# Performance work log

Hardware: AMD Instinct MI355X
Metric: run time of the kernel (lower is better)

The kernel has to match this reference:

```python
import jax, jax.numpy as jnp
import numpy as np
import math

# ---- static config (must match init_kwargs / input_specs) ----
D = 1024
N_HEAD = 16
HEAD_DIM = D // N_HEAD          # 64
HALF = HEAD_DIM // 2            # rope half dim = 32
N_EXP = 8
TOP_K = 2
CAP_FACTOR = 2.0
LN_EPS = 1e-5


def _build_sin_cos(T, half_dim, dtype=jnp.float32):
    pos = jnp.arange(T, dtype=dtype)[:, None]                      # (T,1)
    inv_freq = 1.0 / (10000.0 ** (jnp.arange(0, 2 * half_dim, 2, dtype=dtype) / (2 * half_dim)))
    ang = pos * inv_freq[None, :]                                  # (T, half)
    return jnp.sin(ang), jnp.cos(ang)


def _layernorm(x, g, b):
    mu = jnp.mean(x, axis=-1, keepdims=True)
    var = jnp.mean(jnp.square(x - mu), axis=-1, keepdims=True)
    return (x - mu) * jax.lax.rsqrt(var + LN_EPS) * g + b


def _apply_rope(q, k, sin, cos):
    # q,k: (B,T,H,hd); sin,cos: (T, half)
    s = sin[None, :, None, :]
    c = cos[None, :, None, :]
    q1, q2 = q[..., :HALF], q[..., HALF:]
    k1, k2 = k[..., :HALF], k[..., HALF:]
    qr = jnp.concatenate([q1 * c - q2 * s, q1 * s + q2 * c], axis=-1)
    kr = jnp.concatenate([k1 * c - k2 * s, k1 * s + k2 * c], axis=-1)
    return qr, kr


def _attention(x, Wqkv, Wproj):
    B, T, C = x.shape
    qkv = x @ Wqkv                                                  # (B,T,3C)
    qkv = qkv.reshape(B, T, N_HEAD, 3 * HEAD_DIM)
    q, k, v = jnp.split(qkv, 3, axis=-1)                            # each (B,T,H,hd)
    sin, cos = _build_sin_cos(T, HALF)
    q, k = _apply_rope(q, k, sin, cos)
    scale = 1.0 / math.sqrt(HEAD_DIM)
    att = jnp.einsum('bqhd,bkhd->bhqk', q, k) * scale               # (B,H,T,T)
    causal = jnp.tril(jnp.ones((T, T), dtype=bool))
    att = jnp.where(causal[None, None], att, jnp.finfo(att.dtype).min)
    p = jax.nn.softmax(att, axis=-1)
    o = jnp.einsum('bhqk,bkhd->bqhd', p, v).reshape(B, T, C)
    return o @ Wproj, k, v


def _sparse_moe(flat, Wgate, W1, b1, W2, b2):
    # flat: (N, d). Eval mode: no router noise.
    N, d = flat.shape
    capacity = int(math.ceil(CAP_FACTOR * N / N_EXP))
    logits = flat @ Wgate                                           # (N,E)
    gates = jax.nn.softmax(logits, axis=-1)
    vals, inds = jax.lax.top_k(gates, TOP_K)                        # (N,k)
    flat_inds = inds.reshape(-1)                                    # (N*k,)
    flat_vals = vals.reshape(-1)
    neg = jnp.finfo(flat.dtype).min
    # per-expert assignment scores over all (token, slot) pairs
    scores = jnp.where(flat_inds[None, :] == jnp.arange(N_EXP)[:, None],
                       flat_vals[None, :], neg)                     # (E, N*k)
    top_scores, top_pos = jax.lax.top_k(scores, capacity)           # (E, cap)
    tok_idx = top_pos // TOP_K                                      # (E, cap)
    w = jnp.where(top_scores > neg, top_scores, 0.0)                # dropped slots -> 0 weight
    xe = flat[tok_idx]                                              # gather: (E, cap, d)
    h = jax.nn.gelu(jnp.einsum('ecd,edh->ech', xe, W1) + b1[:, None, :], approximate=False)
    out = jnp.einsum('ech,ehd->ecd', h, W2) + b2[:, None, :]
    out = out * w[..., None]
    final = jnp.zeros_like(flat).at[tok_idx.reshape(-1)].add(out.reshape(-1, d))
    return final


def setup_inputs() -> dict:
    key = jax.random.key(0)
    ks = jax.random.split(key, 10)
    B, T = 2, 2048
    s = 0.02
    return {
        'x': jax.random.normal(ks[0], (B, T, D), dtype=jnp.float32),
        'ln1_g': jnp.ones((D,), jnp.float32),
        'ln1_b': jnp.zeros((D,), jnp.float32),
        'ln2_g': jnp.ones((D,), jnp.float32),
        'ln2_b': jnp.zeros((D,), jnp.float32),
        'Wqkv': jax.random.normal(ks[1], (D, 3 * D), jnp.float32) * s,
        'Wproj': jax.random.normal(ks[2], (D, D), jnp.float32) * s,
        'Wgate': jax.random.normal(ks[3], (D, N_EXP), jnp.float32) * s,
        'W1': jax.random.normal(ks[4], (N_EXP, D, 4 * D), jnp.float32) * s,
        'b1': jnp.zeros((N_EXP, 4 * D), jnp.float32),
        'W2': jax.random.normal(ks[5], (N_EXP, 4 * D, D), jnp.float32) * s,
        'b2': jnp.zeros((N_EXP, D), jnp.float32),
    }


def reference(x, ln1_g, ln1_b, ln2_g, ln2_b, Wqkv, Wproj, Wgate, W1, b1, W2, b2):
    B, T, _ = x.shape
    x_norm = _layernorm(x, ln1_g, ln1_b)
    attn_out, k, v = _attention(x_norm, Wqkv, Wproj)
    x = x + attn_out
    ff_in = _layernorm(x, ln2_g, ln2_b)
    moe_out = _sparse_moe(ff_in.reshape(B * T, D), Wgate, W1, b1, W2, b2)
    x = x + moe_out.reshape(B, T, D)
    aux_loss = jnp.zeros((), x.dtype)  # eval mode
    return x, aux_loss, k, v
```

## Files before the change

kernel.cpp:

```cpp
#include <hip/hip_runtime.h>
#include <hip/hip_bf16.h>
#include <math.h>


#define TT 2048
#define NTOK 4096

typedef __attribute__((ext_vector_type(8))) short bf16x8;
typedef __attribute__((ext_vector_type(4))) float f32x4;
typedef __attribute__((ext_vector_type(16))) float f32x16;

static __device__ __forceinline__ ushort f2bf(float f) {
  union { float f; unsigned u; } v; v.f = f;
  unsigned r = v.u + 0x7FFFu + ((v.u >> 16) & 1u);
  return (ushort)(r >> 16);
}
static __device__ __forceinline__ float bf2f(ushort h) {
  union { unsigned u; float f; } v; v.u = ((unsigned)h) << 16; return v.f;
}
static __device__ __forceinline__ unsigned cvt_pk_bf16(float lo, float hi) {
  unsigned r;
  asm("v_cvt_pk_bf16_f32 %0, %1, %2" : "=v"(r) : "v"(lo), "v"(hi));
  return r;
}
static __device__ __forceinline__ void plane_swap(unsigned& a, unsigned& b) {
  asm("v_permlane32_swap_b32 %0, %1" : "+v"(a), "+v"(b));
}

template<bool WF32>
__global__ __launch_bounds__(256)
void ln_kernel(const float* __restrict__ x, const float* __restrict__ g,
               const float* __restrict__ b, float* __restrict__ out,
               ushort* __restrict__ oh, ushort* __restrict__ ol) {
  int row = blockIdx.x, tid = threadIdx.x;
  const float4* xr = (const float4*)(x + (size_t)row * 1024);
  float4 v = xr[tid];
  float s = v.x + v.y + v.z + v.w;
  #pragma unroll
  for (int off = 1; off < 64; off <<= 1) s += __shfl_xor(s, off);
  __shared__ float red1[4], red2[4];
  if ((tid & 63) == 0) red1[tid >> 6] = s;
  __syncthreads();
  float mu = (red1[0] + red1[1] + red1[2] + red1[3]) * (1.0f / 1024.0f);
  float dx = v.x - mu, dy = v.y - mu, dz = v.z - mu, dw = v.w - mu;
  float ss = dx*dx + dy*dy + dz*dz + dw*dw;
  #pragma unroll
  for (int off = 1; off < 64; off <<= 1) ss += __shfl_xor(ss, off);
  if ((tid & 63) == 0) red2[tid >> 6] = ss;
  __syncthreads();
  float var = (red2[0] + red2[1] + red2[2] + red2[3]) * (1.0f / 1024.0f);
  float inv = 1.0f / sqrtf(var + 1e-5f);
  float4 g4 = ((const float4*)g)[tid];
  float4 b4 = ((const float4*)b)[tid];
  float4 o4;
  o4.x = dx * inv * g4.x + b4.x;
  o4.y = dy * inv * g4.y + b4.y;
  o4.z = dz * inv * g4.z + b4.z;
  o4.w = dw * inv * g4.w + b4.w;
  if constexpr (WF32)
    ((float4*)(out + (size_t)row * 1024))[tid] = o4;
  size_t base = (size_t)row * 1024 + tid * 4;
  ushort h0 = f2bf(o4.x), h1 = f2bf(o4.y), h2 = f2bf(o4.z), h3 = f2bf(o4.w);
  ushort4 hh = {h0, h1, h2, h3};
  *(ushort4*)(oh + base) = hh;
  ushort4 ll = {f2bf(o4.x - bf2f(h0)), f2bf(o4.y - bf2f(h1)),
                f2bf(o4.z - bf2f(h2)), f2bf(o4.w - bf2f(h3))};
  *(ushort4*)(ol + base) = ll;
}

__global__ void sincos_kernel(float* __restrict__ st, float* __restrict__ ct) {
  int t = blockIdx.x, j = threadIdx.x;
  double invf = pow(10000.0, -((double)(2 * j)) / 64.0);
  double ang = (double)t * invf;
  st[t * 32 + j] = (float)sin(ang);
  ct[t * 32 + j] = (float)cos(ang);
}

__global__ __launch_bounds__(256)
void rope_kernel(float* __restrict__ qkv, const float* __restrict__ st,
                 const float* __restrict__ ct, float* __restrict__ kout,
                 float* __restrict__ vout, ushort* __restrict__ Kh,
                 ushort* __restrict__ Kl) {
  int row = blockIdx.x;
  int t = row & (TT - 1);
  int b = row >> 11;
  int tid = threadIdx.x;
  float* base = qkv + (size_t)row * 3072;
  #pragma unroll
  for (int l = 0; l < 2; ++l) {
    int idx = l * 256 + tid;
    int h = idx >> 5, j = idx & 31;
    float s = st[t * 32 + j], c = ct[t * 32 + j];
    float* qp = base + h * 192;
    float q1 = qp[j], q2 = qp[j + 32];
    qp[j]      = q1 * c - q2 * s;
    qp[j + 32] = q1 * s + q2 * c;
    float k1 = qp[64 + j], k2 = qp[96 + j];
    float kr1 = k1 * c - k2 * s, kr2 = k1 * s + k2 * c;
    qp[64 + j] = kr1; qp[96 + j] = kr2;
    kout[(size_t)row * 1024 + h * 64 + j]      = kr1;
    kout[(size_t)row * 1024 + h * 64 + 32 + j] = kr2;
    size_t kb = ((size_t)(b * 16 + h) * TT + t) * 64;
    ushort h1 = f2bf(kr1);
    Kh[kb + j] = h1; Kl[kb + j] = f2bf(kr1 - bf2f(h1));
    ushort h2 = f2bf(kr2);
    Kh[kb + 32 + j] = h2; Kl[kb + 32 + j] = f2bf(kr2 - bf2f(h2));
  }
  #pragma unroll
  for (int l = 0; l < 4; ++l) {
    int f = l * 256 + tid;
    int h = f >> 6, d = f & 63;
    vout[(size_t)row * 1024 + f] = base[h * 192 + 128 + d];
  }
}

__global__ __launch_bounds__(256)
void vtprep_kernel(const float* __restrict__ vout, ushort* __restrict__ Vth,
                   ushort* __restrict__ Vtl) {
  __shared__ float tile[64][65];
  int t0 = blockIdx.x * 64, h = blockIdx.y, b = blockIdx.z;
  int tid = threadIdx.x;
  #pragma unroll
  for (int l = 0; l < 4; ++l) {
    int idx = l * 256 + tid;
    int r = idx >> 4, c4 = (idx & 15) * 4;
    *(float4*)&tile[r][c4] = *(const float4*)&vout[((size_t)(b * TT + t0 + r)) * 1024 + h * 64 + c4];
  }
  __syncthreads();
  int d = tid >> 2, ts = (tid & 3) * 16;
  union { bf16x8 v; ushort u[8]; } H0, H1, L0, L1;
  #pragma unroll
  for (int i = 0; i < 8; ++i) {
    float v0 = tile[ts + i][d];
    ushort hb0 = f2bf(v0);
    H0.u[i] = hb0; L0.u[i] = f2bf(v0 - bf2f(hb0));
    float v1 = tile[ts + 8 + i][d];
    ushort hb1 = f2bf(v1);
    H1.u[i] = hb1; L1.u[i] = f2bf(v1 - bf2f(hb1));
  }
  size_t basep = ((size_t)(b * 16 + h) * 64 + d) * TT + t0 + ts;
  *(bf16x8*)(Vth + basep) = H0.v;  *(bf16x8*)(Vth + basep + 8) = H1.v;
  *(bf16x8*)(Vtl + basep) = L0.v;  *(bf16x8*)(Vtl + basep + 8) = L1.v;
}

__global__ __launch_bounds__(256)
void flash7_kernel(const float* __restrict__ qkv, const ushort* __restrict__ Kh,
                   const ushort* __restrict__ Kl, const ushort* __restrict__ Vth,
                   const ushort* __restrict__ Vtl, float* __restrict__ Opart,
                   float* __restrict__ Mpart, float* __restrict__ Lpart) {
  const int offt[16] = {0,1,2,4,6,9,12,16,20,25,30,36,42,49,56,64};
  int lin = blockIdx.x;
  int xcd = lin & 7, s = lin >> 3;
  int bh = xcd + 8 * (s / 72);
  int j = 71 - (s % 72);
  int qt = 0, off = 0;
  #pragma unroll
  for (int u = 0; u < 16; ++u)
    if (j >= offt[u]) { qt = u; off = offt[u]; }
  int kc = j - off;
  int slot = bh * 72 + j;
  int h = bh & 15, b = bh >> 4;
  int tid = threadIdx.x;
  int w = tid >> 6, lane = tid & 63;
  int q = lane & 31, LH = lane >> 5;
  size_t bT = (size_t)b * TT;
  int qglob0 = qt * 128 + w * 32;
  int qg = qglob0 + q;
  bf16x8 qH[4], qL[4];
  {
    const float* qp = qkv + (bT + qg) * 3072 + h * 192 + LH * 8;
    #pragma unroll
    for (int dblk = 0; dblk < 4; ++dblk) {
      float4 f0 = *(const float4*)(qp + dblk * 16);
      float4 f1 = *(const float4*)(qp + dblk * 16 + 4);
      float vals[8] = {f0.x, f0.y, f0.z, f0.w, f1.x, f1.y, f1.z, f1.w};
      union { bf16x8 v; ushort u[8]; } H, L;
      #pragma unroll
      for (int e = 0; e < 8; ++e) {
        ushort hb = f2bf(vals[e]);
        H.u[e] = hb; L.u[e] = f2bf(vals[e] - bf2f(hb));
      }
      qH[dblk] = H.v; qL[dblk] = L.v;
    }
  }
  const ushort* Kbh = Kh + (size_t)bh * TT * 64;
  const ushort* Kbl = Kl + (size_t)bh * TT * 64;
  const ushort* Vbh = Vth + (size_t)bh * 64 * TT;
  const ushort* Vbl = Vtl + (size_t)bh * 64 * TT;
  f32x16 accO0 = {}, accO1 = {};
  float m = -3.402823466e38f, lsum = 0.0f;
  int kvlo = kc * 256;
  int kvhi = min(kvlo + 256, qglob0 + 32);

  for (int kv0 = kvlo; kv0 < kvhi; kv0 += 32) {
    const ushort* kbh = Kbh + (size_t)(kv0 + q) * 64 + LH * 8;
    const ushort* kbl = Kbl + (size_t)(kv0 + q) * 64 + LH * 8;
    bf16x8 kAH[4], kAL[4];
    #pragma unroll
    for (int dblk = 0; dblk < 4; ++dblk) {
      kAH[dblk] = *(const bf16x8*)(kbh + dblk * 16);
      kAL[dblk] = *(const bf16x8*)(kbl + dblk * 16);
    }
    f32x16 sa = {}, sb = {};
    __builtin_amdgcn_s_setprio(1);
    sa = __builtin_amdgcn_mfma_f32_32x32x16_bf16(kAH[0], qH[0], sa, 0, 0, 0);
    sb = __builtin_amdgcn_mfma_f32_32x32x16_bf16(kAH[2], qH[2], sb, 0, 0, 0);
    sa = __builtin_amdgcn_mfma_f32_32x32x16_bf16(kAH[1], qH[1], sa, 0, 0, 0);
    sb = __builtin_amdgcn_mfma_f32_32x32x16_bf16(kAH[3], qH[3], sb, 0, 0, 0);
    sa = __builtin_amdgcn_mfma_f32_32x32x16_bf16(kAH[0], qL[0], sa, 0, 0, 0);
    sb = __builtin_amdgcn_mfma_f32_32x32x16_bf16(kAH[2], qL[2], sb, 0, 0, 0);
    sa = __builtin_amdgcn_mfma_f32_32x32x16_bf16(kAH[1], qL[1], sa, 0, 0, 0);
    sb = __builtin_amdgcn_mfma_f32_32x32x16_bf16(kAH[3], qL[3], sb, 0, 0, 0);
    sa = __builtin_amdgcn_mfma_f32_32x32x16_bf16(kAL[0], qH[0], sa, 0, 0, 0);
    sb = __builtin_amdgcn_mfma_f32_32x32x16_bf16(kAL[2], qH[2], sb, 0, 0, 0);
    sa = __builtin_amdgcn_mfma_f32_32x32x16_bf16(kAL[1], qH[1], sa, 0, 0, 0);
    sb = __builtin_amdgcn_mfma_f32_32x32x16_bf16(kAL[3], qH[3], sb, 0, 0, 0);
    __builtin_amdgcn_s_setprio(0);
    bf16x8 vAH[2][2], vAL[2][2];
    #pragma unroll
    for (int dblk = 0; dblk < 2; ++dblk)
      #pragma unroll
      for (int s2 = 0; s2 < 2; ++s2) {
        size_t ad = (size_t)(dblk * 32 + q) * TT + kv0 + s2 * 16 + LH * 8;
        vAH[dblk][s2] = *(const bf16x8*)(Vbh + ad);
        vAL[dblk][s2] = *(const bf16x8*)(Vbl + ad);
      }
    float p[16];
    float pmax = -3.402823466e38f;
    if (kv0 + 31 > qglob0) {
      #pragma unroll
      for (int r = 0; r < 16; ++r) {
        int kvg = kv0 + (r & 3) + 8 * (r >> 2) + 4 * LH;
        float sv = (kvg <= qg) ? (sa[r] + sb[r]) * 0.125f : -3.402823466e38f;
        p[r] = sv; pmax = fmaxf(pmax, sv);
      }
    } else {
      #pragma unroll
      for (int r = 0; r < 16; ++r) {
        float sv = (sa[r] + sb[r]) * 0.125f;
        p[r] = sv; pmax = fmaxf(pmax, sv);
      }
    }
    pmax = fmaxf(pmax, __shfl_xor(pmax, 32));
    float mnew = fmaxf(m, pmax);
    float fsc = __expf(m - mnew);
    float psum = 0.0f;
    #pragma unroll
    for (int r = 0; r < 16; ++r) { p[r] = __expf(p[r] - mnew); psum += p[r]; }
    psum += __shfl_xor(psum, 32);
    lsum = lsum * fsc + psum;
    m = mnew;
    #pragma unroll
    for (int r = 0; r < 16; ++r) { accO0[r] *= fsc; accO1[r] *= fsc; }
    bf16x8 pHf[2], pLf[2];
    #pragma unroll
    for (int s2 = 0; s2 < 2; ++s2) {
      int s8 = s2 * 8;
      unsigned a  = cvt_pk_bf16(p[s8 + 0], p[s8 + 1]);
      unsigned bw = cvt_pk_bf16(p[s8 + 2], p[s8 + 3]);
      unsigned c  = cvt_pk_bf16(p[s8 + 4], p[s8 + 5]);
      unsigned d  = cvt_pk_bf16(p[s8 + 6], p[s8 + 7]);
      float l0 = p[s8 + 0] - __uint_as_float(a << 16);
      float l1 = p[s8 + 1] - __uint_as_float(a & 0xFFFF0000u);
      float l2 = p[s8 + 2] - __uint_as_float(bw << 16);
      float l3 = p[s8 + 3] - __uint_as_float(bw & 0xFFFF0000u);
      float l4 = p[s8 + 4] - __uint_as_float(c << 16);
      float l5 = p[s8 + 5] - __uint_as_float(c & 0xFFFF0000u);
      float l6 = p[s8 + 6] - __uint_as_float(d << 16);
      float l7 = p[s8 + 7] - __uint_as_float(d & 0xFFFF0000u);
      unsigned al = cvt_pk_bf16(l0, l1);
      unsigned bl = cvt_pk_bf16(l2, l3);
      unsigned cl = cvt_pk_bf16(l4, l5);
      unsigned dl = cvt_pk_bf16(l6, l7);
      plane_swap(a, c); plane_swap(bw, d);
      plane_swap(al, cl); plane_swap(bl, dl);
      union { unsigned w[4]; bf16x8 v; } PH, PL;
      PH.w[0] = a;  PH.w[1] = bw; PH.w[2] = c;  PH.w[3] = d;
      PL.w[0] = al; PL.w[1] = bl; PL.w[2] = cl; PL.w[3] = dl;
      pHf[s2] = PH.v; pLf[s2] = PL.v;
    }
    __builtin_amdgcn_s_setprio(1);
    #pragma unroll
    for (int s2 = 0; s2 < 2; ++s2) {
      accO0 = __builtin_amdgcn_mfma_f32_32x32x16_bf16(vAH[0][s2], pHf[s2], accO0, 0, 0, 0);
      accO1 = __builtin_amdgcn_mfma_f32_32x32x16_bf16(vAH[1][s2], pHf[s2], accO1, 0, 0, 0);
      accO0 = __builtin_amdgcn_mfma_f32_32x32x16_bf16(vAH[0][s2], pLf[s2], accO0, 0, 0, 0);
      accO1 = __builtin_amdgcn_mfma_f32_32x32x16_bf16(vAH[1][s2], pLf[s2], accO1, 0, 0, 0);
      accO0 = __builtin_amdgcn_mfma_f32_32x32x16_bf16(vAL[0][s2], pHf[s2], accO0, 0, 0, 0);
      accO1 = __builtin_amdgcn_mfma_f32_32x32x16_bf16(vAL[1][s2], pHf[s2], accO1, 0, 0, 0);
    }
    __builtin_amdgcn_s_setprio(0);
  }
  if (LH == 0) {
    Mpart[slot * 128 + w * 32 + q] = m;
    Lpart[slot * 128 + w * 32 + q] = lsum;
  }
  float* Ob = Opart + (size_t)slot * 8192 + (w * 32 + q) * 64;
  #pragma unroll
  for (int g2 = 0; g2 < 4; ++g2) {
    float4 v0 = {accO0[g2 * 4 + 0], accO0[g2 * 4 + 1], accO0[g2 * 4 + 2], accO0[g2 * 4 + 3]};
    *(float4*)(Ob + 8 * g2 + 4 * LH) = v0;
    float4 v1 = {accO1[g2 * 4 + 0], accO1[g2 * 4 + 1], accO1[g2 * 4 + 2], accO1[g2 * 4 + 3]};
    *(float4*)(Ob + 32 + 8 * g2 + 4 * LH) = v1;
  }
}

__global__ __launch_bounds__(256)
void fmerge2_kernel(const float* __restrict__ Opart, const float* __restrict__ Mpart,
                    const float* __restrict__ Lpart, ushort* __restrict__ oh,
                    ushort* __restrict__ ol) {
  const int offt[16] = {0,1,2,4,6,9,12,16,20,25,30,36,42,49,56,64};
  int qt = blockIdx.x, bh = blockIdx.y;
  int h = bh & 15, b = bh >> 4;
  int nc = (qt + 2) >> 1;
  int slot0 = bh * 72 + offt[qt];
  int tid = threadIdx.x;
  int q = tid & 127, dh = tid >> 7;
  float mg = -3.402823466e38f;
  for (int c = 0; c < nc; ++c) mg = fmaxf(mg, Mpart[(slot0 + c) * 128 + q]);
  float lg = 0.0f;
  float4 acc[8] = {};
  for (int c = 0; c < nc; ++c) {
    float sc = __expf(Mpart[(slot0 + c) * 128 + q] - mg);
    lg += sc * Lpart[(slot0 + c) * 128 + q];
    const float4* op = (const float4*)(Opart + (size_t)(slot0 + c) * 8192 + q * 64 + dh * 32);
    #pragma unroll
    for (int i = 0; i < 8; ++i) {
      float4 v = op[i];
      acc[i].x += sc * v.x; acc[i].y += sc * v.y;
      acc[i].z += sc * v.z; acc[i].w += sc * v.w;
    }
  }
  float inv = 1.0f / lg;
  size_t obase = ((size_t)(b * TT + qt * 128 + q)) * 1024 + h * 64 + dh * 32;
  #pragma unroll
  for (int i = 0; i < 8; ++i) {
    float4 v = {acc[i].x * inv, acc[i].y * inv, acc[i].z * inv, acc[i].w * inv};
    ushort h0 = f2bf(v.x), h1 = f2bf(v.y), h2 = f2bf(v.z), h3 = f2bf(v.w);
    ushort4 hh = {h0, h1, h2, h3};
    *(ushort4*)(oh + obase + i * 4) = hh;
    ushort4 ll = {f2bf(v.x - bf2f(h0)), f2bf(v.y - bf2f(h1)),
                  f2bf(v.z - bf2f(h2)), f2bf(v.w - bf2f(h3))};
    *(ushort4*)(ol + obase + i * 4) = ll;
  }
}

template<bool LO>
__global__ void tconv_kernel(const float* __restrict__ in, ushort* __restrict__ oh,
                             ushort* __restrict__ ol, int K, int N) {
  __shared__ float t[32][33];
  int z = blockIdx.z;
  const float* ip = in + (size_t)z * K * N;
  ushort* ohp = oh + (size_t)z * K * N;
  ushort* olp = LO ? (ol + (size_t)z * K * N) : nullptr;
  int n0 = blockIdx.x * 32, k0 = blockIdx.y * 32;
  int tx = threadIdx.x, ty = threadIdx.y;
  #pragma unroll
  for (int i = 0; i < 4; ++i)
    t[ty + 8 * i][tx] = ip[(size_t)(k0 + ty + 8 * i) * N + n0 + tx];
  __syncthreads();
  #pragma unroll
  for (int i = 0; i < 4; ++i) {
    float v = t[tx][ty + 8 * i];
    size_t off = (size_t)(n0 + ty + 8 * i) * K + k0 + tx;
    ushort hb = f2bf(v);
    ohp[off] = hb;
    if (LO) olp[off] = f2bf(v - bf2f(hb));
  }
}

#define LOAD_STEP(tt) do {                                                     \
    int seg = SPLIT3 ? ((tt) / kPer) : 0;                                      \
    int kk = (SPLIT3 ? ((tt) % kPer) : (tt)) << 6;                             \
    const ushort* Ause = (SPLIT3 && seg == 2) ? AlB : AhB;                     \
    const ushort* Buse = (SPLIT3 && seg == 1) ? BlB : BhB;                     \
    _Pragma("unroll")                                                          \
    for (int q = 0; q < 4; ++q) {                                              \
      int rr = r0 + 32 * q;                                                    \
      int clog = cph ^ (rr & 7);                                               \
      ra[q] = *(const bf16x8*)(Ause + (size_t)garow[q] * K + kk + clog * 8);   \
      rb[q] = *(const bf16x8*)(Buse + (size_t)(bn + rr) * K + kk + clog * 8);  \
    }                                                                          \
  } while (0)

template<int EPI, bool GATHER, bool SPLIT3>
__global__ __launch_bounds__(256, 2)
void mgemm(const ushort* __restrict__ Ah, const ushort* __restrict__ Al,
           const ushort* __restrict__ Bh, const ushort* __restrict__ Bl,
           void* __restrict__ Cv, const float* __restrict__ extra,
           const int* __restrict__ gatAll, int N, int K,
           long aEStride, long bEStride, long cEStride, int biasEStride) {
  __shared__ ushort As[128 * 64];
  __shared__ ushort Bs[128 * 64];
  int z = blockIdx.z;
  const ushort* AhB = Ah + (size_t)z * aEStride;
  const ushort* AlB = SPLIT3 ? (Al + (size_t)z * aEStride) : nullptr;
  const ushort* BhB = Bh + (size_t)z * bEStride;
  const ushort* BlB = SPLIT3 ? (Bl + (size_t)z * bEStride) : nullptr;
  const int* gat = GATHER ? (gatAll + z * 1024) : nullptr;
  int bm = blockIdx.y * 128, bn = blockIdx.x * 128;
  int tid = threadIdx.x;
  int r0 = tid >> 3, cph = tid & 7;
  int garow[4];
  #pragma unroll
  for (int q = 0; q < 4; ++q) {
    int rr = r0 + 32 * q;
    garow[q] = GATHER ? gat[bm + rr] : (bm + rr);
  }
  int kPer = K >> 6;
  int kSteps = (SPLIT3 ? 3 : 1) * kPer;
  int wid = tid >> 6, lane = tid & 63;
  int wm = wid >> 1, wn = wid & 1;
  int lr = lane & 15, lk = lane >> 4;
  f32x4 acc[4][4] = {};
  bf16x8 ra[4], rb[4];
  LOAD_STEP(0);
  for (int t = 0; t < kSteps; ++t) {
    __syncthreads();
    #pragma unroll
    for (int q = 0; q < 4; ++q) {
      int rr = r0 + 32 * q;
      *(bf16x8*)&As[rr * 64 + cph * 8] = ra[q];
      *(bf16x8*)&Bs[rr * 64 + cph * 8] = rb[q];
    }
    __syncthreads();
    if (t + 1 < kSteps) LOAD_STEP(t + 1);
    #pragma unroll
    for (int kh = 0; kh < 2; ++kh) {
      bf16x8 af[4], bfr[4];
      #pragma unroll
      for (int mf = 0; mf < 4; ++mf) {
        int row = wm * 64 + mf * 16 + lr;
        int ch = (kh * 4 + lk) ^ (row & 7);
        af[mf] = *(const bf16x8*)&As[row * 64 + ch * 8];
      }
      #pragma unroll
      for (int nf = 0; nf < 4; ++nf) {
        int row = wn * 64 + nf * 16 + lr;
        int ch = (kh * 4 + lk) ^ (row & 7);
        bfr[nf] = *(const bf16x8*)&Bs[row * 64 + ch * 8];
      }
      #pragma unroll
      for (int mf = 0; mf < 4; ++mf)
        #pragma unroll
        for (int nf = 0; nf < 4; ++nf)
          acc[mf][nf] = __builtin_amdgcn_mfma_f32_16x16x32_bf16(af[mf], bfr[nf], acc[mf][nf], 0, 0, 0);
    }
  }
  int crow = bm + wm * 64, ccol = bn + wn * 64;
  if constexpr (EPI <= 1) {
    float* C = (float*)Cv;
    #pragma unroll
    for (int mf = 0; mf < 4; ++mf)
      #pragma unroll
      for (int nf = 0; nf < 4; ++nf)
        #pragma unroll
        for (int r = 0; r < 4; ++r) {
          int row = crow + mf * 16 + lk * 4 + r;
          int col = ccol + nf * 16 + lr;
          float v = acc[mf][nf][r];
          if constexpr (EPI == 1) v += extra[(size_t)row * N + col];
          C[(size_t)row * N + col] = v;
        }
  } else {
    const float* bias = extra + (size_t)z * biasEStride;
    ushort* C = (ushort*)Cv + (size_t)z * cEStride;
    #pragma unroll
    for (int mf = 0; mf < 4; ++mf)
      #pragma unroll
      for (int nf = 0; nf < 4; ++nf)
        #pragma unroll
        for (int r = 0; r < 4; ++r) {
          int row = crow + mf * 16 + lk * 4 + r;
          int col = ccol + nf * 16 + lr;
          float v = acc[mf][nf][r] + bias[col];
          if constexpr (EPI == 2)
            v = 0.5f * v * (1.0f + erff(v * 0.70710678118654752f));
          C[(size_t)row * N + col] = f2bf(v);
        }
  }
}

__global__ __launch_bounds__(256)
void gate_kernel(const float* __restrict__ ffin, const float* __restrict__ Wg,
                 int* __restrict__ te, float* __restrict__ tv, int* __restrict__ inv) {
  int token = blockIdx.x, tid = threadIdx.x;
  float acc[8] = {};
  const float* xr = ffin + (size_t)token * 1024;
  for (int i = tid; i < 1024; i += 256) {
    float xv = xr[i];
    const float4* wr = (const float4*)&Wg[i * 8];
    float4 w0 = wr[0], w1 = wr[1];
    acc[0] += xv * w0.x; acc[1] += xv * w0.y; acc[2] += xv * w0.z; acc[3] += xv * w0.w;
    acc[4] += xv * w1.x; acc[5] += xv * w1.y; acc[6] += xv * w1.z; acc[7] += xv * w1.w;
  }
  #pragma unroll
  for (int off = 1; off < 64; off <<= 1)
    #pragma unroll
    for (int q = 0; q < 8; ++q) acc[q] += __shfl_xor(acc[q], off);
  __shared__ float red[4][8];
  if ((tid & 63) == 0)
    #pragma unroll
    for (int q = 0; q < 8; ++q) red[tid >> 6][q] = acc[q];
  __syncthreads();
  if (tid == 0) {
    float g[8];
    #pragma unroll
    for (int q = 0; q < 8; ++q) g[q] = red[0][q] + red[1][q] + red[2][q] + red[3][q];
    float mx = g[0];
    #pragma unroll
    for (int q = 1; q < 8; ++q) mx = fmaxf(mx, g[q]);
    float sum = 0.0f;
    #pragma unroll
    for (int q = 0; q < 8; ++q) { g[q] = expf(g[q] - mx); sum += g[q]; }
    float inv_s = 1.0f / sum;
    #pragma unroll
    for (int q = 0; q < 8; ++q) g[q] *= inv_s;
    int e1 = 0; float v1 = g[0];
    for (int q = 1; q < 8; ++q) if (g[q] > v1) { v1 = g[q]; e1 = q; }
    int e2 = -1; float v2 = -1.0f;
    for (int q = 0; q < 8; ++q) { if (q == e1) continue; if (g[q] > v2) { v2 = g[q]; e2 = q; } }
    te[token * 2] = e1; te[token * 2 + 1] = e2;
    tv[token * 2] = v1; tv[token * 2 + 1] = v2;
    inv[token * 2] = -1; inv[token * 2 + 1] = -1;
  }
}

__global__ __launch_bounds__(1024)
void route_sort_kernel(const int* __restrict__ te, const float* __restrict__ tv,
                       int* __restrict__ etok, float* __restrict__ ew,
                       int* __restrict__ inv) {
  __shared__ unsigned long long sk[4096];
  __shared__ int wcnt[16];
  __shared__ int base;
  int e = blockIdx.x, tid = threadIdx.x;
  int lane = tid & 63, wv = tid >> 6;
  if (tid == 0) base = 0;
  __syncthreads();
  for (int c = 0; c < 8; ++c) {
    int s = c * 1024 + tid;
    bool sel = (te[s] == e);
    unsigned long long ball = __ballot(sel);
    int pre = __popcll(ball & ((1ull << lane) - 1ull));
    if (lane == 0) wcnt[wv] = __popcll(ball);
    __syncthreads();
    int woff = 0, tot = 0;
    #pragma unroll
    for (int i = 0; i < 16; ++i) {
      int cc = wcnt[i];
      if (i < wv) woff += cc;
      tot += cc;
    }
    if (sel) {
      unsigned vb = __float_as_uint(tv[s]);
      sk[base + woff + pre] =
          ((unsigned long long)vb << 32) | (unsigned)(0xFFFFFFFFu - (unsigned)s);
    }
    __syncthreads();
    if (tid == 0) base += tot;
    __syncthreads();
  }
  int n = base;
  if (n > 1024) {
    int P = (n <= 2048) ? 2048 : 4096;
    for (int i = n + tid; i < P; i += 1024) sk[i] = 0ull;
    __syncthreads();
    for (int k = 2; k <= P; k <<= 1)
      for (int j = k >> 1; j > 0; j >>= 1) {
        for (int t = tid; t < (P >> 1); t += 1024) {
          int i = ((t & ~(j - 1)) << 1) | (t & (j - 1));
          int p = i | j;
          unsigned long long a = sk[i], bq = sk[p];
          bool desc = ((i & k) == 0);
          if (desc ? (a < bq) : (a > bq)) { sk[i] = bq; sk[p] = a; }
        }
        __syncthreads();
      }
  }
  int cap = n < 1024 ? n : 1024;
  if (tid < cap) {
    unsigned long long key = sk[tid];
    unsigned slot = 0xFFFFFFFFu - (unsigned)(key & 0xFFFFFFFFull);
    etok[e * 1024 + tid] = (int)(slot >> 1);
    ew[e * 1024 + tid] = __uint_as_float((unsigned)(key >> 32));
    inv[slot] = e * 1024 + tid;
  } else {
    etok[e * 1024 + tid] = 0;
    ew[e * 1024 + tid] = 0.0f;
  }
}

__global__ __launch_bounds__(256)
void combine_kernel(const float* __restrict__ xres, const ushort* __restrict__ eo,
                    const int* __restrict__ inv, const float* __restrict__ ew,
                    float* __restrict__ outx, float* __restrict__ aux) {
  int token = blockIdx.x;
  int d = threadIdx.x * 4;
  float4 acc = *(const float4*)&xres[(size_t)token * 1024 + d];
  #pragma unroll
  for (int j = 0; j < 2; ++j) {
    int p = inv[token * 2 + j];
    if (p >= 0) {
      float w = ew[p];
      const ushort* ep = eo + (size_t)p * 1024 + d;
      acc.x += w * bf2f(ep[0]); acc.y += w * bf2f(ep[1]);
      acc.z += w * bf2f(ep[2]); acc.w += w * bf2f(ep[3]);
    }
  }
  *(float4*)&outx[(size_t)token * 1024 + d] = acc;
  if (token == 0 && threadIdx.x == 0) aux[0] = 0.0f;
}

extern "C" void kernel_launch(void* const* d_in, const int* in_sizes, int n_in,
                              void* d_out, int out_size, void* d_ws, size_t ws_size,
                              hipStream_t stream) {
  const float* x     = (const float*)d_in[0];
  const float* ln1g  = (const float*)d_in[1];
  const float* ln1b  = (const float*)d_in[2];
  const float* ln2g  = (const float*)d_in[3];
  const float* ln2b  = (const float*)d_in[4];
  const float* Wqkv  = (const float*)d_in[5];
  const float* Wproj = (const float*)d_in[6];
  const float* Wg    = (const float*)d_in[7];
  const float* W1    = (const float*)d_in[8];
  const float* b1    = (const float*)d_in[9];
  const float* W2    = (const float*)d_in[10];
  const float* b2    = (const float*)d_in[11];

  float* out_x   = (float*)d_out;
  float* out_aux = out_x + 4194304;
  float* out_k   = out_aux + 1;
  float* out_v   = out_k + 4194304;

  float* ws   = (float*)d_ws;
  float* A    = ws;
  float* qkvb = ws + 4194304;
  float* o    = ws + 16777216;
  float* st   = ws + 20971520;
  float* ct   = ws + 21037056;
  int*   te   = (int*)(ws + 21102592);
  float* tv   = ws + 21110784;
  int*   etok = (int*)(ws + 21118976);
  float* ew   = ws + 21127168;
  int*   inv  = (int*)(ws + 21135360);
  ushort* bfAh = (ushort*)(ws + 21143552);
  ushort* bfAl = (ushort*)(ws + 23240704);
  ushort* BqH  = (ushort*)(ws + 25337856);
  ushort* BqL  = (ushort*)(ws + 26910720);
  ushort* BpH  = (ushort*)(ws + 28483584);
  ushort* BpL  = (ushort*)(ws + 29007872);
  ushort* W1t  = (ushort*)(ws + 29532160);
  ushort* W2t  = (ushort*)(ws + 46309376);
  ushort* eo   = (ushort*)(ws + 63086592);
  ushort* hbuf = (ushort*)(ws + 4194304);
  ushort* Kh_  = bfAh;
  ushort* Kl_  = bfAl;
  ushort* Vth_ = eo;
  ushort* Vtl_ = eo + 4194304;
  float* Opart = ws + 29532160;
  float* Mpart = ws + 48406528;
  float* Lpart = ws + 48701440;

  tconv_kernel<true ><<<dim3(96, 32, 1),  dim3(32, 8), 0, stream>>>(Wqkv,  BqH, BqL, 1024, 3072);
  tconv_kernel<true ><<<dim3(32, 32, 1),  dim3(32, 8), 0, stream>>>(Wproj, BpH, BpL, 1024, 1024);
  sincos_kernel<<<TT, 32, 0, stream>>>(st, ct);

  ln_kernel<false><<<NTOK, 256, 0, stream>>>(x, ln1g, ln1b, nullptr, bfAh, bfAl);
  mgemm<0, false, true><<<dim3(24, 32, 1), 256, 0, stream>>>(
      bfAh, bfAl, BqH, BqL, qkvb, nullptr, nullptr, 3072, 1024, 0, 0, 0, 0);
  rope_kernel<<<NTOK, 256, 0, stream>>>(qkvb, st, ct, out_k, out_v, Kh_, Kl_);
  vtprep_kernel<<<dim3(32, 16, 2), 256, 0, stream>>>(out_v, Vth_, Vtl_);
  flash7_kernel<<<2304, 256, 0, stream>>>(qkvb, Kh_, Kl_, Vth_, Vtl_, Opart, Mpart, Lpart);
  fmerge2_kernel<<<dim3(16, 32), 256, 0, stream>>>(Opart, Mpart, Lpart, bfAh, bfAl);
  mgemm<1, false, true><<<dim3(8, 32, 1), 256, 0, stream>>>(
      bfAh, bfAl, BpH, BpL, A, x, nullptr, 1024, 1024, 0, 0, 0, 0);
  tconv_kernel<false><<<dim3(128, 32, 8), dim3(32, 8), 0, stream>>>(W1, W1t, nullptr, 1024, 4096);
  tconv_kernel<false><<<dim3(32, 128, 8), dim3(32, 8), 0, stream>>>(W2, W2t, nullptr, 4096, 1024);
  ln_kernel<true><<<NTOK, 256, 0, stream>>>(A, ln2g, ln2b, o, bfAh, bfAl);
  gate_kernel<<<NTOK, 256, 0, stream>>>(o, Wg, te, tv, inv);
  route_sort_kernel<<<8, 1024, 0, stream>>>(te, tv, etok, ew, inv);
  mgemm<2, true, false><<<dim3(32, 8, 8), 256, 0, stream>>>(
      bfAh, nullptr, W1t, nullptr, hbuf, b1, etok, 4096, 1024,
      0, 4096L * 1024, 1024L * 4096, 4096);
  mgemm<3, false, false><<<dim3(8, 8, 8), 256, 0, stream>>>(
      hbuf, nullptr, W2t, nullptr, eo, b2, nullptr, 1024, 4096,
      1024L * 4096, 1024L * 4096, 1024L * 1024, 1024);
  combine_kernel<<<NTOK, 256, 0, stream>>>(A, eo, inv, ew, out_x, out_aux);
}
```

Measured before the change: 704.0 us.

## Fuse MoE gate into second layernorm and software-pipeline K loads in flash attention

The router gate computation (logits, softmax, top-2) moves into the second layernorm kernel, working on the normalized row held in shared memory. This removes the fp32 layernorm output write, its re-read and one kernel launch. The flash kernel now prefetches the next K tile into a second register set while the current tile's MFMAs run, and folds the 1/sqrt(d) scale into Q before bf16 splitting. This costs extra registers and may lower occupancy, and pre-scaling Q changes rounding slightly (0.125 is exact, so the effect should be small).

```diff
diff --git a/kernel.cpp b/kernel.cpp
--- a/kernel.cpp
+++ b/kernel.cpp
@@ -27,11 +27,13 @@
   asm("v_permlane32_swap_b32 %0, %1" : "+v"(a), "+v"(b));
 }
 
-template<bool WF32>
+template<bool GATE>
 __global__ __launch_bounds__(256)
 void ln_kernel(const float* __restrict__ x, const float* __restrict__ g,
-               const float* __restrict__ b, float* __restrict__ out,
-               ushort* __restrict__ oh, ushort* __restrict__ ol) {
+               const float* __restrict__ b, ushort* __restrict__ oh,
+               ushort* __restrict__ ol, const float* __restrict__ Wg,
+               int* __restrict__ te, float* __restrict__ tv, int* __restrict__ inv) {
+  __shared__ float srow[1024];
   int row = blockIdx.x, tid = threadIdx.x;
   const float4* xr = (const float4*)(x + (size_t)row * 1024);
   float4 v = xr[tid];
@@ -49,16 +51,14 @@
   if ((tid & 63) == 0) red2[tid >> 6] = ss;
   __syncthreads();
   float var = (red2[0] + red2[1] + red2[2] + red2[3]) * (1.0f / 1024.0f);
-  float inv = 1.0f / sqrtf(var + 1e-5f);
+  float inv_ = 1.0f / sqrtf(var + 1e-5f);
   float4 g4 = ((const float4*)g)[tid];
   float4 b4 = ((const float4*)b)[tid];
   float4 o4;
-  o4.x = dx * inv * g4.x + b4.x;
-  o4.y = dy * inv * g4.y + b4.y;
-  o4.z = dz * inv * g4.z + b4.z;
-  o4.w = dw * inv * g4.w + b4.w;
-  if constexpr (WF32)
-    ((float4*)(out + (size_t)row * 1024))[tid] = o4;
+  o4.x = dx * inv_ * g4.x + b4.x;
+  o4.y = dy * inv_ * g4.y + b4.y;
+  o4.z = dz * inv_ * g4.z + b4.z;
+  o4.w = dw * inv_ * g4.w + b4.w;
   size_t base = (size_t)row * 1024 + tid * 4;
   ushort h0 = f2bf(o4.x), h1 = f2bf(o4.y), h2 = f2bf(o4.z), h3 = f2bf(o4.w);
   ushort4 hh = {h0, h1, h2, h3};
@@ -66,6 +66,48 @@
   ushort4 ll = {f2bf(o4.x - bf2f(h0)), f2bf(o4.y - bf2f(h1)),
                 f2bf(o4.z - bf2f(h2)), f2bf(o4.w - bf2f(h3))};
   *(ushort4*)(ol + base) = ll;
+  if constexpr (GATE) {
+    *(float4*)&srow[tid * 4] = o4;
+    __syncthreads();
+    float acc[8] = {};
+    for (int i = tid; i < 1024; i += 256) {
+      float xv = srow[i];
+      const float4* wr = (const float4*)&Wg[i * 8];
+      float4 w0 = wr[0], w1 = wr[1];
+      acc[0] += xv * w0.x; acc[1] += xv * w0.y; acc[2] += xv * w0.z; acc[3] += xv * w0.w;
+      acc[4] += xv * w1.x; acc[5] += xv * w1.y; acc[6] += xv * w1.z; acc[7] += xv * w1.w;
+    }
+    #pragma unroll
+    for (int off = 1; off < 64; off <<= 1)
+      #pragma unroll
+      for (int qq = 0; qq < 8; ++qq) acc[qq] += __shfl_xor(acc[qq], off);
+    __shared__ float red[4][8];
+    if ((tid & 63) == 0)
+      #pragma unroll
+      for (int qq = 0; qq < 8; ++qq) red[tid >> 6][qq] = acc[qq];
+    __syncthreads();
+    if (tid == 0) {
+      float gg[8];
+      #pragma unroll
+      for (int qq = 0; qq < 8; ++qq) gg[qq] = red[0][qq] + red[1][qq] + red[2][qq] + red[3][qq];
+      float mx = gg[0];
+      #pragma unroll
+      for (int qq = 1; qq < 8; ++qq) mx = fmaxf(mx, gg[qq]);
+      float sum = 0.0f;
+      #pragma unroll
+      for (int qq = 0; qq < 8; ++qq) { gg[qq] = expf(gg[qq] - mx); sum += gg[qq]; }
+      float inv_s = 1.0f / sum;
+      #pragma unroll
+      for (int qq = 0; qq < 8; ++qq) gg[qq] *= inv_s;
+      int e1 = 0; float v1 = gg[0];
+      for (int qq = 1; qq < 8; ++qq) if (gg[qq] > v1) { v1 = gg[qq]; e1 = qq; }
+      int e2 = -1; float v2 = -1.0f;
+      for (int qq = 0; qq < 8; ++qq) { if (qq == e1) continue; if (gg[qq] > v2) { v2 = gg[qq]; e2 = qq; } }
+      te[row * 2] = e1; te[row * 2 + 1] = e2;
+      tv[row * 2] = v1; tv[row * 2 + 1] = v2;
+      inv[row * 2] = -1; inv[row * 2 + 1] = -1;
+    }
+  }
 }
 
 __global__ void sincos_kernel(float* __restrict__ st, float* __restrict__ ct) {
@@ -144,7 +186,7 @@
 }
 
 __global__ __launch_bounds__(256)
-void flash7_kernel(const float* __restrict__ qkv, const ushort* __restrict__ Kh,
+void flash8_kernel(const float* __restrict__ qkv, const ushort* __restrict__ Kh,
                    const ushort* __restrict__ Kl, const ushort* __restrict__ Vth,
                    const ushort* __restrict__ Vtl, float* __restrict__ Opart,
                    float* __restrict__ Mpart, float* __restrict__ Lpart) {
@@ -173,7 +215,8 @@
     for (int dblk = 0; dblk < 4; ++dblk) {
       float4 f0 = *(const float4*)(qp + dblk * 16);
       float4 f1 = *(const float4*)(qp + dblk * 16 + 4);
-      float vals[8] = {f0.x, f0.y, f0.z, f0.w, f1.x, f1.y, f1.z, f1.w};
+      float vals[8] = {f0.x * 0.125f, f0.y * 0.125f, f0.z * 0.125f, f0.w * 0.125f,
+                       f1.x * 0.125f, f1.y * 0.125f, f1.z * 0.125f, f1.w * 0.125f};
       union { bf16x8 v; ushort u[8]; } H, L;
       #pragma unroll
       for (int e = 0; e < 8; ++e) {
@@ -192,30 +235,18 @@
   int kvlo = kc * 256;
   int kvhi = min(kvlo + 256, qglob0 + 32);
 
-  for (int kv0 = kvlo; kv0 < kvhi; kv0 += 32) {
+  auto loadK = [&](bf16x8 (&kH)[4], bf16x8 (&kL)[4], int kv0) {
     const ushort* kbh = Kbh + (size_t)(kv0 + q) * 64 + LH * 8;
     const ushort* kbl = Kbl + (size_t)(kv0 + q) * 64 + LH * 8;
-    bf16x8 kAH[4], kAL[4];
     #pragma unroll
     for (int dblk = 0; dblk < 4; ++dblk) {
-      kAH[dblk] = *(const bf16x8*)(kbh + dblk * 16);
-      kAL[dblk] = *(const bf16x8*)(kbl + dblk * 16);
-    }
-    f32x16 sa = {}, sb = {};
-    __builtin_amdgcn_s_setprio(1);
-    sa = __builtin_amdgcn_mfma_f32_32x32x16_bf16(kAH[0], qH[0], sa, 0, 0, 0);
-    sb = __builtin_amdgcn_mfma_f32_32x32x16_bf16(kAH[2], qH[2], sb, 0, 0, 0);
-    sa = __builtin_amdgcn_mfma_f32_32x32x16_bf16(kAH[1], qH[1], sa, 0, 0, 0);
-    sb = __builtin_amdgcn_mfma_f32_32x32x16_bf16(kAH[3], qH[3], sb, 0, 0, 0);
-    sa = __builtin_amdgcn_mfma_f32_32x32x16_bf16(kAH[0], qL[0], sa, 0, 0, 0);
-    sb = __builtin_amdgcn_mfma_f32_32x32x16_bf16(kAH[2], qL[2], sb, 0, 0, 0);
-    sa = __builtin_amdgcn_mfma_f32_32x32x16_bf16(kAH[1], qL[1], sa, 0, 0, 0);
-    sb = __builtin_amdgcn_mfma_f32_32x32x16_bf16(kAH[3], qL[3], sb, 0, 0, 0);
-    sa = __builtin_amdgcn_mfma_f32_32x32x16_bf16(kAL[0], qH[0], sa, 0, 0, 0);
-    sb = __builtin_amdgcn_mfma_f32_32x32x16_bf16(kAL[2], qH[2], sb, 0, 0, 0);
-    sa = __builtin_amdgcn_mfma_f32_32x32x16_bf16(kAL[1], qH[1], sa, 0, 0, 0);
-    sb = __builtin_amdgcn_mfma_f32_32x32x16_bf16(kAL[3], qH[3], sb, 0, 0, 0);
-    __builtin_amdgcn_s_setprio(0);
+      kH[dblk] = *(const bf16x8*)(kbh + dblk * 16);
+      kL[dblk] = *(const bf16x8*)(kbl + dblk * 16);
+    }
+  };
+
+  auto tile = [&](bf16x8 (&kH)[4], bf16x8 (&kL)[4],
+                  bf16x8 (&kHn)[4], bf16x8 (&kLn)[4], int kv0, bool pf) {
     bf16x8 vAH[2][2], vAL[2][2];
     #pragma unroll
     for (int dblk = 0; dblk < 2; ++dblk)
@@ -225,19 +256,35 @@
         vAH[dblk][s2] = *(const bf16x8*)(Vbh + ad);
         vAL[dblk][s2] = *(const bf16x8*)(Vbl + ad);
       }
+    f32x16 sa = {}, sb = {};
+    __builtin_amdgcn_s_setprio(1);
+    sa = __builtin_amdgcn_mfma_f32_32x32x16_bf16(kH[0], qH[0], sa, 0, 0, 0);
+    sb = __builtin_amdgcn_mfma_f32_32x32x16_bf16(kH[2], qH[2], sb, 0, 0, 0);
+    sa = __builtin_amdgcn_mfma_f32_32x32x16_bf16(kH[1], qH[1], sa, 0, 0, 0);
+    sb = __builtin_amdgcn_mfma_f32_32x32x16_bf16(kH[3], qH[3], sb, 0, 0, 0);
+    sa = __builtin_amdgcn_mfma_f32_32x32x16_bf16(kH[0], qL[0], sa, 0, 0, 0);
+    sb = __builtin_amdgcn_mfma_f32_32x32x16_bf16(kH[2], qL[2], sb, 0, 0, 0);
+    sa = __builtin_amdgcn_mfma_f32_32x32x16_bf16(kH[1], qL[1], sa, 0, 0, 0);
+    sb = __builtin_amdgcn_mfma_f32_32x32x16_bf16(kH[3], qL[3], sb, 0, 0, 0);
+    sa = __builtin_amdgcn_mfma_f32_32x32x16_bf16(kL[0], qH[0], sa, 0, 0, 0);
+    sb = __builtin_amdgcn_mfma_f32_32x32x16_bf16(kL[2], qH[2], sb, 0, 0, 0);
+    sa = __builtin_amdgcn_mfma_f32_32x32x16_bf16(kL[1], qH[1], sa, 0, 0, 0);
+    sb = __builtin_amdgcn_mfma_f32_32x32x16_bf16(kL[3], qH[3], sb, 0, 0, 0);
+    __builtin_amdgcn_s_setprio(0);
+    if (pf) loadK(kHn, kLn, kv0 + 32);
     float p[16];
     float pmax = -3.402823466e38f;
     if (kv0 + 31 > qglob0) {
       #pragma unroll
       for (int r = 0; r < 16; ++r) {
         int kvg = kv0 + (r & 3) + 8 * (r >> 2) + 4 * LH;
-        float sv = (kvg <= qg) ? (sa[r] + sb[r]) * 0.125f : -3.402823466e38f;
+        float sv = (kvg <= qg) ? (sa[r] + sb[r]) : -3.402823466e38f;
         p[r] = sv; pmax = fmaxf(pmax, sv);
       }
     } else {
       #pragma unroll
       for (int r = 0; r < 16; ++r) {
-        float sv = (sa[r] + sb[r]) * 0.125f;
+        float sv = sa[r] + sb[r];
         p[r] = sv; pmax = fmaxf(pmax, sv);
       }
     }
@@ -290,7 +337,16 @@
       accO1 = __builtin_amdgcn_mfma_f32_32x32x16_bf16(vAL[1][s2], pHf[s2], accO1, 0, 0, 0);
     }
     __builtin_amdgcn_s_setprio(0);
-  }
+  };
+
+  bf16x8 kA[4], kB[4], kC[4], kD[4];
+  loadK(kA, kB, kvlo);
+  for (int kv0 = kvlo; kv0 < kvhi; kv0 += 64) {
+    tile(kA, kB, kC, kD, kv0, kv0 + 32 < kvhi);
+    if (kv0 + 32 < kvhi)
+      tile(kC, kD, kA, kB, kv0 + 32, kv0 + 64 < kvhi);
+  }
+
   if (LH == 0) {
     Mpart[slot * 128 + w * 32 + q] = m;
     Lpart[slot * 128 + w * 32 + q] = lsum;
@@ -481,51 +537,6 @@
   }
 }
 
-__global__ __launch_bounds__(256)
-void gate_kernel(const float* __restrict__ ffin, const float* __restrict__ Wg,
-                 int* __restrict__ te, float* __restrict__ tv, int* __restrict__ inv) {
-  int token = blockIdx.x, tid = threadIdx.x;
-  float acc[8] = {};
-  const float* xr = ffin + (size_t)token * 1024;
-  for (int i = tid; i < 1024; i += 256) {
-    float xv = xr[i];
-    const float4* wr = (const float4*)&Wg[i * 8];
-    float4 w0 = wr[0], w1 = wr[1];
-    acc[0] += xv * w0.x; acc[1] += xv * w0.y; acc[2] += xv * w0.z; acc[3] += xv * w0.w;
-    acc[4] += xv * w1.x; acc[5] += xv * w1.y; acc[6] += xv * w1.z; acc[7] += xv * w1.w;
-  }
-  #pragma unroll
-  for (int off = 1; off < 64; off <<= 1)
-    #pragma unroll
-    for (int q = 0; q < 8; ++q) acc[q] += __shfl_xor(acc[q], off);
-  __shared__ float red[4][8];
-  if ((tid & 63) == 0)
-    #pragma unroll
-    for (int q = 0; q < 8; ++q) red[tid >> 6][q] = acc[q];
-  __syncthreads();
-  if (tid == 0) {
-    float g[8];
-    #pragma unroll
-    for (int q = 0; q < 8; ++q) g[q] = red[0][q] + red[1][q] + red[2][q] + red[3][q];
-    float mx = g[0];
-    #pragma unroll
-    for (int q = 1; q < 8; ++q) mx = fmaxf(mx, g[q]);
-    float sum = 0.0f;
-    #pragma unroll
-    for (int q = 0; q < 8; ++q) { g[q] = expf(g[q] - mx); sum += g[q]; }
-    float inv_s = 1.0f / sum;
-    #pragma unroll
-    for (int q = 0; q < 8; ++q) g[q] *= inv_s;
-    int e1 = 0; float v1 = g[0];
-    for (int q = 1; q < 8; ++q) if (g[q] > v1) { v1 = g[q]; e1 = q; }
-    int e2 = -1; float v2 = -1.0f;
-    for (int q = 0; q < 8; ++q) { if (q == e1) continue; if (g[q] > v2) { v2 = g[q]; e2 = q; } }
-    te[token * 2] = e1; te[token * 2 + 1] = e2;
-    tv[token * 2] = v1; tv[token * 2 + 1] = v2;
-    inv[token * 2] = -1; inv[token * 2 + 1] = -1;
-  }
-}
-
 __global__ __launch_bounds__(1024)
 void route_sort_kernel(const int* __restrict__ te, const float* __restrict__ tv,
                        int* __restrict__ etok, float* __restrict__ ew,
@@ -635,7 +646,6 @@
   float* ws   = (float*)d_ws;
   float* A    = ws;
   float* qkvb = ws + 4194304;
-  float* o    = ws + 16777216;
   float* st   = ws + 20971520;
   float* ct   = ws + 21037056;
   int*   te   = (int*)(ws + 21102592);
@@ -665,19 +675,19 @@
   tconv_kernel<true ><<<dim3(32, 32, 1),  dim3(32, 8), 0, stream>>>(Wproj, BpH, BpL, 1024, 1024);
   sincos_kernel<<<TT, 32, 0, stream>>>(st, ct);
 
-  ln_kernel<false><<<NTOK, 256, 0, stream>>>(x, ln1g, ln1b, nullptr, bfAh, bfAl);
+  ln_kernel<false><<<NTOK, 256, 0, stream>>>(x, ln1g, ln1b, bfAh, bfAl,
+                                             nullptr, nullptr, nullptr, nullptr);
   mgemm<0, false, true><<<dim3(24, 32, 1), 256, 0, stream>>>(
       bfAh, bfAl, BqH, BqL, qkvb, nullptr, nullptr, 3072, 1024, 0, 0, 0, 0);
   rope_kernel<<<NTOK, 256, 0, stream>>>(qkvb, st, ct, out_k, out_v, Kh_, Kl_);
   vtprep_kernel<<<dim3(32, 16, 2), 256, 0, stream>>>(out_v, Vth_, Vtl_);
-  flash7_kernel<<<2304, 256, 0, stream>>>(qkvb, Kh_, Kl_, Vth_, Vtl_, Opart, Mpart, Lpart);
+  flash8_kernel<<<2304, 256, 0, stream>>>(qkvb, Kh_, Kl_, Vth_, Vtl_, Opart, Mpart, Lpart);
   fmerge2_kernel<<<dim3(16, 32), 256, 0, stream>>>(Opart, Mpart, Lpart, bfAh, bfAl);
   mgemm<1, false, true><<<dim3(8, 32, 1), 256, 0, stream>>>(
       bfAh, bfAl, BpH, BpL, A, x, nullptr, 1024, 1024, 0, 0, 0, 0);
   tconv_kernel<false><<<dim3(128, 32, 8), dim3(32, 8), 0, stream>>>(W1, W1t, nullptr, 1024, 4096);
   tconv_kernel<false><<<dim3(32, 128, 8), dim3(32, 8), 0, stream>>>(W2, W2t, nullptr, 4096, 1024);
-  ln_kernel<true><<<NTOK, 256, 0, stream>>>(A, ln2g, ln2b, o, bfAh, bfAl);
-  gate_kernel<<<NTOK, 256, 0, stream>>>(o, Wg, te, tv, inv);
+  ln_kernel<true><<<NTOK, 256, 0, stream>>>(A, ln2g, ln2b, bfAh, bfAl, Wg, te, tv, inv);
   route_sort_kernel<<<8, 1024, 0, stream>>>(te, tv, etok, ew, inv);
   mgemm<2, true, false><<<dim3(32, 8, 8), 256, 0, stream>>>(
       bfAh, nullptr, W1t, nullptr, hbuf, b1, etok, 4096, 1024,
```

New measurement: 694.9 us. About the same (-1.3%).
